# Kernel optimization log

Measured on AMD Instinct MI355X. Metric: run time of the kernel, lower is better.

## Reference

```python
import jax, jax.numpy as jnp
import numpy as np

B, S, M, E, H = 4, 2048, 1024, 8, 4096
CAP = 2 * (B * S) // E  # GShard top-2 capacity = 2*s/e = 2048


def setup_inputs() -> dict:
    key = jax.random.key(0)
    k = jax.random.split(key, 6)
    sc = 0.02
    return {
        "x": jax.random.normal(k[0], (B, S, M), jnp.float32),
        "wg": jax.random.normal(k[1], (M, E), jnp.float32) * sc,
        "w1": jax.random.normal(k[2], (E, M, H), jnp.float32) * sc,
        "b1": jnp.zeros((E, H), jnp.float32),
        "w2": jax.random.normal(k[3], (E, H, M), jnp.float32) * sc,
        "b2": jnp.zeros((E, M), jnp.float32),
    }


def top2gating(logits, capacity):
    # Faithful GShard/fairscale top2gating: logits [s, e]
    s, e = logits.shape
    gates = jax.nn.softmax(logits, axis=-1)
    idx1 = jnp.argmax(gates, axis=1)
    mask1 = jax.nn.one_hot(idx1, e, dtype=jnp.float32)
    logits2 = jnp.where(mask1 > 0, -jnp.inf, logits)
    idx2 = jnp.argmax(logits2, axis=1)
    mask2 = jax.nn.one_hot(idx2, e, dtype=jnp.float32)
    # positions within each expert's buffer
    loc1 = jnp.cumsum(mask1, axis=0) - 1.0
    loc2 = jnp.cumsum(mask2, axis=0) - 1.0 + jnp.sum(mask1, axis=0, keepdims=True)
    # load-balancing aux loss (computed before capacity drop, per fairscale)
    me = jnp.mean(gates, axis=0)
    ce = jnp.mean(mask1, axis=0)
    l_aux = jnp.mean(me * ce) * (e * e)
    # drop tokens over capacity
    mask1 = mask1 * (loc1 < capacity)
    mask2 = mask2 * (loc2 < capacity)
    loc1_s = jnp.sum(loc1 * mask1, axis=1).astype(jnp.int32)
    loc2_s = jnp.sum(loc2 * mask2, axis=1).astype(jnp.int32)
    gates1 = jnp.sum(gates * mask1, axis=1)
    gates2 = jnp.sum(gates * mask2, axis=1)
    denom = jnp.maximum(gates1 + gates2, 1e-9)
    gates1 = gates1 / denom
    gates2 = gates2 / denom
    # dense [s, e, c] combine weights (as in the original einsum formulation)
    oh1 = jax.nn.one_hot(loc1_s, capacity, dtype=jnp.float32)
    oh2 = jax.nn.one_hot(loc2_s, capacity, dtype=jnp.float32)
    combine = (gates1[:, None] * mask1)[:, :, None] * oh1[:, None, :] \
            + (gates2[:, None] * mask2)[:, :, None] * oh2[:, None, :]
    dispatch = combine > 0
    return l_aux, combine, dispatch


def reference(x, wg, w1, b1, w2, b2):
    d_model = x.shape[2]
    xf = x.reshape(-1, d_model)                      # [s, m]
    logits = xf @ wg                                 # [s, e]
    l_aux, combine, dispatch = top2gating(logits, CAP)
    # dispatch: dense one-hot scatter, as in torch.einsum('sec,sm->ecm')
    disp = jnp.einsum('sec,sm->ecm', dispatch.astype(xf.dtype), xf)
    # per-expert FFN (Linear -> ReLU -> Linear), vectorized over experts
    h = jax.nn.relu(jnp.einsum('ecm,emh->ech', disp, w1) + b1[:, None, :])
    eo = jnp.einsum('ech,ehm->ecm', h, w2) + b2[:, None, :]
    # combine: torch.einsum('sec,ecm->sm')
    out = jnp.einsum('sec,ecm->sm', combine, eo)
    return out.reshape(x.shape), l_aux
```

## Files before the change

kernel.cpp:

```cpp
#include <hip/hip_runtime.h>
#include <stdint.h>

typedef unsigned short u16;
typedef __attribute__((ext_vector_type(8))) short bf16x8;
typedef __attribute__((ext_vector_type(4))) float f32x4;

#define TOKENS 8192
#define DM 1024
#define NE 8
#define DH 4096
#define CAP 2048

__device__ __forceinline__ u16 f2bf(float f) {
  unsigned int u = __float_as_uint(f);
  u = u + 0x7FFFu + ((u >> 16) & 1u);
  return (u16)(u >> 16);
}

__device__ __forceinline__ void gll16(const void* g, void* l) {
  __builtin_amdgcn_global_load_lds(
      (const __attribute__((address_space(1))) unsigned int*)g,
      (__attribute__((address_space(3))) unsigned int*)l, 16, 0, 0);
}

__global__ __launch_bounds__(256) void gating_kernel(
    const float* __restrict__ x, const float* __restrict__ wg,
    int* __restrict__ idx1, int* __restrict__ idx2,
    float* __restrict__ g1r, float* __restrict__ g2r, float* __restrict__ me) {
  __shared__ float gsh[4][8];
  int lane = threadIdx.x & 63;
  int w = threadIdx.x >> 6;
  int t = blockIdx.x * 4 + w;
  const float* xr = x + (size_t)t * DM;
  double acc[8];
#pragma unroll
  for (int e = 0; e < 8; ++e) acc[e] = 0.0;
#pragma unroll
  for (int it = 0; it < 4; ++it) {
    float4 xv = ((const float4*)xr)[it * 64 + lane];
    int base = (it * 64 + lane) * 4;
    const float* wr = wg + (size_t)base * 8;
    float xs[4] = {xv.x, xv.y, xv.z, xv.w};
#pragma unroll
    for (int j = 0; j < 4; ++j)
#pragma unroll
      for (int e = 0; e < 8; ++e) acc[e] += (double)xs[j] * (double)wr[j * 8 + e];
  }
#pragma unroll
  for (int off = 32; off > 0; off >>= 1)
#pragma unroll
    for (int e = 0; e < 8; ++e) acc[e] += __shfl_down(acc[e], off);
  if (lane == 0) {
    float l[8];
#pragma unroll
    for (int e = 0; e < 8; ++e) l[e] = (float)acc[e];
    int i1 = 0;
    float v1 = l[0];
#pragma unroll
    for (int e = 1; e < 8; ++e)
      if (l[e] > v1) { v1 = l[e]; i1 = e; }
    int i2 = -1;
    float v2 = -3.4e38f;
#pragma unroll
    for (int e = 0; e < 8; ++e)
      if (e != i1 && l[e] > v2) { v2 = l[e]; i2 = e; }
    float s = 0.f;
    float p[8];
#pragma unroll
    for (int e = 0; e < 8; ++e) { p[e] = expf(l[e] - v1); s += p[e]; }
    float inv = 1.f / s;
    idx1[t] = i1;
    idx2[t] = i2;
    g1r[t] = inv;
    g2r[t] = expf(v2 - v1) * inv;
#pragma unroll
    for (int e = 0; e < 8; ++e) gsh[w][e] = p[e] * inv;
  }
  __syncthreads();
  if (threadIdx.x < 8) {
    int e = threadIdx.x;
    atomicAdd(&me[e], gsh[0][e] + gsh[1][e] + gsh[2][e] + gsh[3][e]);
  }
}

__global__ __launch_bounds__(1024) void scan_kernel(
    const int* __restrict__ idx1, const int* __restrict__ idx2,
    const float* __restrict__ g1r, const float* __restrict__ g2r,
    const float* __restrict__ me,
    int* __restrict__ slot1, int* __restrict__ slot2,
    float* __restrict__ g1n, float* __restrict__ g2n,
    int* __restrict__ slot2tok, float* __restrict__ laux) {
  __shared__ u16 c[16][1024];
  __shared__ u16 csum[16][32];
  __shared__ int tot[16];
  int tid = threadIdx.x;
  int i1[8], i2[8];
#pragma unroll
  for (int ctr = 0; ctr < 16; ++ctr) c[ctr][tid] = 0;
#pragma unroll
  for (int j = 0; j < 8; ++j) {
    int t = tid * 8 + j;
    i1[j] = idx1[t];
    i2[j] = idx2[t];
    c[i1[j]][tid]++;
    c[8 + i2[j]][tid]++;
  }
  __syncthreads();
  if (tid < 512) {
    int ctr = tid >> 5, ch = tid & 31;
    int s = 0;
#pragma unroll
    for (int i = 0; i < 32; ++i) s += c[ctr][ch * 32 + i];
    csum[ctr][ch] = (u16)s;
  }
  __syncthreads();
  if (tid < 16) {
    int run = 0;
#pragma unroll
    for (int ch = 0; ch < 32; ++ch) {
      int v = csum[tid][ch];
      csum[tid][ch] = (u16)run;
      run += v;
    }
    tot[tid] = run;
  }
  __syncthreads();
  if (tid < 512) {
    int ctr = tid >> 5, ch = tid & 31;
    int run = csum[ctr][ch];
#pragma unroll
    for (int i = 0; i < 32; ++i) {
      int v = c[ctr][ch * 32 + i];
      c[ctr][ch * 32 + i] = (u16)run;
      run += v;
    }
  }
  __syncthreads();
#pragma unroll
  for (int j = 0; j < 8; ++j) {
    int t = tid * 8 + j;
    int e1 = i1[j], e2 = i2[j];
    int L1 = c[e1][tid]++;
    int L2 = c[8 + e2][tid]++;
    L2 += tot[e2];
    bool kv1 = L1 < CAP, kv2 = L2 < CAP;
    float G1 = kv1 ? g1r[t] : 0.f;
    float G2 = kv2 ? g2r[t] : 0.f;
    float den = fmaxf(G1 + G2, 1e-9f);
    g1n[t] = G1 / den;
    g2n[t] = G2 / den;
    int s1 = kv1 ? (e1 * CAP + L1) : -1;
    int s2 = kv2 ? (e2 * CAP + L2) : -1;
    slot1[t] = s1;
    slot2[t] = s2;
    if (kv1) slot2tok[s1] = t;
    if (kv2) slot2tok[s2] = t;
  }
  if (tid == 0) {
    double a = 0.0;
    for (int e = 0; e < 8; ++e)
      a += ((double)me[e] / 8192.0) * ((double)tot[e] / 8192.0);
    laux[0] = (float)(a * 8.0);
  }
}

__global__ void transpose_kernel(const float* __restrict__ src, u16* __restrict__ dst,
                                 int R, int C) {
  __shared__ float tile[32][33];
  int tx = threadIdx.x, ty = threadIdx.y;
  int r0 = blockIdx.y * 32, c0 = blockIdx.x * 32;
  const float* s = src + (size_t)blockIdx.z * R * C;
  u16* d = dst + (size_t)blockIdx.z * R * C;
#pragma unroll
  for (int i = 0; i < 32; i += 8) tile[ty + i][tx] = s[(size_t)(r0 + ty + i) * C + c0 + tx];
  __syncthreads();
#pragma unroll
  for (int i = 0; i < 32; i += 8)
    d[(size_t)(c0 + ty + i) * R + r0 + tx] = f2bf(tile[tx][ty + i]);
}

__global__ void gather_kernel(const float* __restrict__ x, const int* __restrict__ slot2tok,
                              u16* __restrict__ xe) {
  int slot = blockIdx.y * CAP + blockIdx.x;
  int tok = slot2tok[slot];
  int tid = threadIdx.x;
  u16 o[8];
  if (tok >= 0) {
    const float4* xr = (const float4*)(x + (size_t)tok * DM);
    float4 a = xr[tid * 2], b = xr[tid * 2 + 1];
    o[0] = f2bf(a.x); o[1] = f2bf(a.y); o[2] = f2bf(a.z); o[3] = f2bf(a.w);
    o[4] = f2bf(b.x); o[5] = f2bf(b.y); o[6] = f2bf(b.z); o[7] = f2bf(b.w);
  } else {
#pragma unroll
    for (int j = 0; j < 8; ++j) o[j] = 0;
  }
  *(uint4*)(xe + (size_t)slot * DM + tid * 8) = *(const uint4*)o;
}

#define BAR()                              \
  {                                        \
    asm volatile("" ::: "memory");         \
    __builtin_amdgcn_s_barrier();          \
    asm volatile("" ::: "memory");         \
  }
#define VMCNT(n) asm volatile("s_waitcnt vmcnt(" #n ")" ::: "memory")

template <int RELU, int OUTBF16>
__global__ __launch_bounds__(512, 2) void gemm_kernel(
    const u16* __restrict__ A, const u16* __restrict__ Bt,
    const float* __restrict__ bias, void* __restrict__ Cv,
    int MO, int NO, int K) {
  __shared__ __align__(16) u16 As[2][256 * 64];
  __shared__ __align__(16) u16 Bs[2][256 * 64];
  const int tid = threadIdx.x;
  const int lane = tid & 63, wid = tid >> 6;
  const int wm = wid >> 2, wn = wid & 3;

  const int gx = gridDim.x, gy = gridDim.y;
  const int nwg = gx * gy * gridDim.z;
  const int L = (blockIdx.z * gy + blockIdx.y) * gx + blockIdx.x;
  const int cpx = nwg >> 3;
  const int Ls = (L & 7) * cpx + (L >> 3);
  const int bx = Ls % gx;
  const int tq = Ls / gx;
  const int by = tq % gy;
  const int eb = tq / gy;

  const size_t Ks2 = (size_t)K * 2;
  const char* Ag = (const char*)(A + (size_t)eb * MO * K + (size_t)by * 256 * K);
  const char* Bg = (const char*)(Bt + (size_t)eb * NO * K + (size_t)bx * 256 * K);
  const int rl = tid >> 3;
  const int sb = ((tid & 7) * 16) ^ ((rl & 7) << 4);
  Ag += (size_t)rl * Ks2 + sb;
  Bg += (size_t)rl * Ks2 + sb;
  char* AsB = ((char*)As) + tid * 16;
  char* BsB = ((char*)Bs) + tid * 16;
  const u16* AsE = &As[0][0];
  const u16* BsE = &Bs[0][0];
  const int fr = lane & 15, kg8 = (lane >> 4) * 8;
  const int swz = (fr & 7) << 3;

#define STAGE_A(BUF_, REG_, KT_) \
  gll16(Ag + (size_t)((REG_)*64) * Ks2 + (size_t)(KT_)*128, AsB + (BUF_)*32768 + (REG_)*8192)
#define STAGE_B(BUF_, REG_, KT_) \
  gll16(Bg + (size_t)((REG_)*64) * Ks2 + (size_t)(KT_)*128, BsB + (BUF_)*32768 + (REG_)*8192)
#define LDA(BUF_, M_, K_) \
  (*(const bf16x8*)&AsE[(BUF_)*16384 + (wm * 128 + (M_)*16 + fr) * 64 + (((K_)*32 + kg8) ^ swz)])
#define LDB(BUF_, N_, K_) \
  (*(const bf16x8*)&BsE[(BUF_)*16384 + (wn * 64 + (N_)*16 + fr) * 64 + (((K_)*32 + kg8) ^ swz)])
#define MFMA_Q(MB_, NB_)                                                            \
  _Pragma("unroll") for (int k = 0; k < 2; ++k)                                     \
  _Pragma("unroll") for (int m = 0; m < 4; ++m)                                     \
  _Pragma("unroll") for (int n = 0; n < 2; ++n)                                     \
      acc[(MB_) + m][(NB_) + n] = __builtin_amdgcn_mfma_f32_16x16x32_bf16(          \
          areg[m][k], breg[(NB_) + n][k], acc[(MB_) + m][(NB_) + n], 0, 0, 0)

  f32x4 acc[8][4];
#pragma unroll
  for (int i = 0; i < 8; ++i)
#pragma unroll
    for (int j = 0; j < 4; ++j) acc[i][j] = {0.f, 0.f, 0.f, 0.f};
  bf16x8 areg[4][2], breg[4][2];

  const int NT = K >> 6;

#define TILE_STEP(CUR_, NXT_, ST_)                                                  \
  {                                                                                 \
                          \
    STAGE_A(NXT_, 0, ST_); STAGE_A(NXT_, 1, ST_);                                   \
    STAGE_A(NXT_, 2, ST_); STAGE_A(NXT_, 3, ST_);                                   \
    STAGE_B(NXT_, 0, ST_); STAGE_B(NXT_, 1, ST_);                                   \
    STAGE_B(NXT_, 2, ST_); STAGE_B(NXT_, 3, ST_);                                   \
                                   \
    _Pragma("unroll") for (int m = 0; m < 4; ++m) {                                 \
      areg[m][0] = LDA(CUR_, m, 0); areg[m][1] = LDA(CUR_, m, 1);                   \
    }                                                                               \
    _Pragma("unroll") for (int n = 0; n < 4; ++n) {                                 \
      breg[n][0] = LDB(CUR_, n, 0); breg[n][1] = LDB(CUR_, n, 1);                   \
    }                                                                               \
    __builtin_amdgcn_s_setprio(1);                                                  \
    MFMA_Q(0, 0); MFMA_Q(0, 2);                                                     \
    __builtin_amdgcn_s_setprio(0);                                                  \
                          \
    _Pragma("unroll") for (int m = 0; m < 4; ++m) {                                 \
      areg[m][0] = LDA(CUR_, 4 + m, 0); areg[m][1] = LDA(CUR_, 4 + m, 1);           \
    }                                                                               \
    __builtin_amdgcn_s_setprio(1);                                                  \
    MFMA_Q(4, 0); MFMA_Q(4, 2);                                                     \
    __builtin_amdgcn_s_setprio(0);                                                  \
    VMCNT(0);           \
    BAR();              \
  }

  STAGE_A(0, 0, 0); STAGE_A(0, 1, 0); STAGE_A(0, 2, 0); STAGE_A(0, 3, 0);
  STAGE_B(0, 0, 0); STAGE_B(0, 1, 0); STAGE_B(0, 2, 0); STAGE_B(0, 3, 0);
  VMCNT(0);
  BAR();

  for (int t = 0; t < NT; t += 2) {
    const int s1 = (t + 1 < NT) ? t + 1 : NT - 1;
    const int s2 = (t + 2 < NT) ? t + 2 : NT - 1;
    TILE_STEP(0, 1, s1);
    TILE_STEP(1, 0, s2);
  }

  const int row0 = by * 256 + wm * 128 + (kg8 >> 3) * 4;
  const int col0 = bx * 256 + wn * 64 + fr;
  const float* be = bias + (size_t)eb * NO;
  size_t cbase = (size_t)eb * MO * NO;
#pragma unroll
  for (int m = 0; m < 8; ++m) {
#pragma unroll
    for (int n = 0; n < 4; ++n) {
      int col = col0 + n * 16;
      float bv = be[col];
#pragma unroll
      for (int r = 0; r < 4; ++r) {
        int row = row0 + m * 16 + r;
        float v = acc[m][n][r] + bv;
        if (RELU) v = fmaxf(v, 0.f);
        if (OUTBF16)
          ((u16*)Cv)[cbase + (size_t)row * NO + col] = f2bf(v);
        else
          ((float*)Cv)[cbase + (size_t)row * NO + col] = v;
      }
    }
  }
#undef TILE_STEP
#undef STAGE_A
#undef STAGE_B
#undef LDA
#undef LDB
#undef MFMA_Q
}

__global__ void combine_kernel(const float* __restrict__ eo,
                               const float* __restrict__ g1n, const float* __restrict__ g2n,
                               const int* __restrict__ slot1, const int* __restrict__ slot2,
                               float* __restrict__ out) {
  int t = blockIdx.x, tid = threadIdx.x;
  float g1 = g1n[t], g2 = g2n[t];
  int s1 = slot1[t], s2 = slot2[t];
  float4 o = make_float4(0.f, 0.f, 0.f, 0.f);
  if (s1 >= 0) {
    float4 a = ((const float4*)(eo + (size_t)s1 * DM))[tid];
    o.x = g1 * a.x; o.y = g1 * a.y; o.z = g1 * a.z; o.w = g1 * a.w;
  }
  if (s2 >= 0) {
    float4 b = ((const float4*)(eo + (size_t)s2 * DM))[tid];
    o.x += g2 * b.x; o.y += g2 * b.y; o.z += g2 * b.z; o.w += g2 * b.w;
  }
  ((float4*)(out + (size_t)t * DM))[tid] = o;
}

extern "C" void kernel_launch(void* const* d_in, const int* in_sizes, int n_in,
                              void* d_out, int out_size, void* d_ws, size_t ws_size,
                              hipStream_t stream) {
  const float* x = (const float*)d_in[0];
  const float* wg = (const float*)d_in[1];
  const float* w1 = (const float*)d_in[2];
  const float* b1 = (const float*)d_in[3];
  const float* w2 = (const float*)d_in[4];
  const float* b2 = (const float*)d_in[5];
  float* out = (float*)d_out;

  const size_t SZ_WT1 = (size_t)NE * DH * DM * 2;
  const size_t SZ_WT2 = (size_t)NE * DM * DH * 2;
  const size_t SZ_XE = (size_t)NE * CAP * DM * 2;
  const size_t SZ_H = (size_t)NE * CAP * DH * 2;
  const size_t SZ_TOK = (size_t)TOKENS * 4;

  char* p = (char*)d_ws;
  u16* wt1 = (u16*)p;
  float* eo = (float*)p;            p += SZ_WT1;
  u16* wt2 = (u16*)p;               p += SZ_WT2;
  u16* xe = (u16*)p;                p += SZ_XE;
  u16* h = (u16*)p;                 p += SZ_H;
  int* idx1 = (int*)p;              p += SZ_TOK;
  int* idx2 = (int*)p;              p += SZ_TOK;
  int* slot1 = (int*)p;             p += SZ_TOK;
  int* slot2 = (int*)p;             p += SZ_TOK;
  float* g1r = (float*)p;           p += SZ_TOK;
  float* g2r = (float*)p;           p += SZ_TOK;
  float* g1n = (float*)p;           p += SZ_TOK;
  float* g2n = (float*)p;           p += SZ_TOK;
  int* slot2tok = (int*)p;          p += (size_t)NE * CAP * 4;
  float* me = (float*)p;            p += 256;
  if ((size_t)(p - (char*)d_ws) > ws_size) return;

  hipMemsetAsync(me, 0, 32, stream);
  hipMemsetAsync(slot2tok, 0xFF, (size_t)NE * CAP * 4, stream);

  gating_kernel<<<TOKENS / 4, 256, 0, stream>>>(x, wg, idx1, idx2, g1r, g2r, me);
  scan_kernel<<<1, 1024, 0, stream>>>(idx1, idx2, g1r, g2r, me, slot1, slot2, g1n, g2n,
                                      slot2tok, out + (size_t)TOKENS * DM);
  transpose_kernel<<<dim3(DH / 32, DM / 32, NE), dim3(32, 8), 0, stream>>>(w1, wt1, DM, DH);
  transpose_kernel<<<dim3(DM / 32, DH / 32, NE), dim3(32, 8), 0, stream>>>(w2, wt2, DH, DM);
  gather_kernel<<<dim3(CAP, NE), 128, 0, stream>>>(x, slot2tok, xe);
  gemm_kernel<1, 1><<<dim3(DH / 256, CAP / 256, NE), 512, 0, stream>>>(xe, wt1, b1, (void*)h,
                                                                       CAP, DH, DM);
  gemm_kernel<0, 0><<<dim3(DM / 256, CAP / 256, NE), 512, 0, stream>>>(h, wt2, b2, (void*)eo,
                                                                       CAP, DM, DH);
  combine_kernel<<<TOKENS, 256, 0, stream>>>(eo, g1n, g2n, slot1, slot2, out);
}
```

Baseline: 461.6 us.

## Interleave global-to-LDS staging with MFMA quarters in a finer-grained ping-pong schedule

Replaces the per-tile stage-all-then-compute step with an 8-phase schedule. Each quarter of MFMA work is bracketed by barriers and lgkmcnt waits, and the next tile's A/B sub-blocks are issued piecewise between quarters. Part of the next buffer is prefetched up front, so global loads stay in flight across compute with partial vmcnt waits instead of a full drain each tile. This aims to hide load latency and smooth memory traffic, at the cost of many more barriers per tile and fragile hand-counted wait thresholds.

```diff
diff --git a/kernel.cpp b/kernel.cpp
--- a/kernel.cpp
+++ b/kernel.cpp
@@ -204,6 +204,7 @@
     asm volatile("" ::: "memory");         \
   }
 #define VMCNT(n) asm volatile("s_waitcnt vmcnt(" #n ")" ::: "memory")
+#define LGKM(n) asm volatile("s_waitcnt lgkmcnt(" #n ")" ::: "memory")
 
 template <int RELU, int OUTBF16>
 __global__ __launch_bounds__(512, 2) void gemm_kernel(
@@ -255,6 +256,31 @@
       acc[(MB_) + m][(NB_) + n] = __builtin_amdgcn_mfma_f32_16x16x32_bf16(          \
           areg[m][k], breg[(NB_) + n][k], acc[(MB_) + m][(NB_) + n], 0, 0, 0)
 
+#define RD_A03(C_)                                                \
+  _Pragma("unroll") for (int m = 0; m < 4; ++m) {                 \
+    areg[m][0] = LDA(C_, m, 0); areg[m][1] = LDA(C_, m, 1);       \
+  }
+#define RD_A47(C_)                                                \
+  _Pragma("unroll") for (int m = 0; m < 4; ++m) {                 \
+    areg[m][0] = LDA(C_, 4 + m, 0); areg[m][1] = LDA(C_, 4 + m, 1); \
+  }
+#define RD_B01(C_)                                                \
+  _Pragma("unroll") for (int n = 0; n < 2; ++n) {                 \
+    breg[n][0] = LDB(C_, n, 0); breg[n][1] = LDB(C_, n, 1);       \
+  }
+#define RD_B23(C_)                                                \
+  _Pragma("unroll") for (int n = 2; n < 4; ++n) {                 \
+    breg[n][0] = LDB(C_, n, 0); breg[n][1] = LDB(C_, n, 1);       \
+  }
+#define MM(MB_, NB_)                          \
+  BAR();                                      \
+  LGKM(0);                                    \
+  __builtin_amdgcn_sched_barrier(0);          \
+  __builtin_amdgcn_s_setprio(1);              \
+  MFMA_Q(MB_, NB_);                           \
+  __builtin_amdgcn_s_setprio(0);              \
+  BAR();
+
   f32x4 acc[8][4];
 #pragma unroll
   for (int i = 0; i < 8; ++i)
@@ -264,44 +290,43 @@
 
   const int NT = K >> 6;
 
-#define TILE_STEP(CUR_, NXT_, ST_)                                                  \
-  {                                                                                 \
-                          \
-    STAGE_A(NXT_, 0, ST_); STAGE_A(NXT_, 1, ST_);                                   \
-    STAGE_A(NXT_, 2, ST_); STAGE_A(NXT_, 3, ST_);                                   \
-    STAGE_B(NXT_, 0, ST_); STAGE_B(NXT_, 1, ST_);                                   \
-    STAGE_B(NXT_, 2, ST_); STAGE_B(NXT_, 3, ST_);                                   \
-                                   \
-    _Pragma("unroll") for (int m = 0; m < 4; ++m) {                                 \
-      areg[m][0] = LDA(CUR_, m, 0); areg[m][1] = LDA(CUR_, m, 1);                   \
-    }                                                                               \
-    _Pragma("unroll") for (int n = 0; n < 4; ++n) {                                 \
-      breg[n][0] = LDB(CUR_, n, 0); breg[n][1] = LDB(CUR_, n, 1);                   \
-    }                                                                               \
-    __builtin_amdgcn_s_setprio(1);                                                  \
-    MFMA_Q(0, 0); MFMA_Q(0, 2);                                                     \
-    __builtin_amdgcn_s_setprio(0);                                                  \
-                          \
-    _Pragma("unroll") for (int m = 0; m < 4; ++m) {                                 \
-      areg[m][0] = LDA(CUR_, 4 + m, 0); areg[m][1] = LDA(CUR_, 4 + m, 1);           \
-    }                                                                               \
-    __builtin_amdgcn_s_setprio(1);                                                  \
-    MFMA_Q(4, 0); MFMA_Q(4, 2);                                                     \
-    __builtin_amdgcn_s_setprio(0);                                                  \
-    VMCNT(0);           \
-    BAR();              \
-  }
-
   STAGE_A(0, 0, 0); STAGE_A(0, 1, 0); STAGE_A(0, 2, 0); STAGE_A(0, 3, 0);
   STAGE_B(0, 0, 0); STAGE_B(0, 1, 0); STAGE_B(0, 2, 0); STAGE_B(0, 3, 0);
-  VMCNT(0);
+  STAGE_A(1, 0, 1); STAGE_A(1, 2, 1);
+  STAGE_B(1, 0, 1); STAGE_B(1, 1, 1);
+  STAGE_B(1, 2, 1); STAGE_B(1, 3, 1);
+  VMCNT(6);
   BAR();
 
   for (int t = 0; t < NT; t += 2) {
-    const int s1 = (t + 1 < NT) ? t + 1 : NT - 1;
-    const int s2 = (t + 2 < NT) ? t + 2 : NT - 1;
-    TILE_STEP(0, 1, s1);
-    TILE_STEP(1, 0, s2);
+    const int t2 = (t + 2 < NT) ? t + 2 : NT - 2;
+    const int t3 = (t + 3 < NT) ? t + 3 : NT - 1;
+    RD_A03(0); RD_B01(0);
+    STAGE_A(1, 1, t + 1); STAGE_A(1, 3, t + 1);
+    LGKM(8);
+    MM(0, 0);
+    RD_B23(0);
+    STAGE_A(0, 0, t2); STAGE_A(0, 2, t2);
+    MM(0, 2);
+    RD_A47(0);
+    STAGE_B(0, 0, t2); STAGE_B(0, 1, t2);
+    MM(4, 0);
+    STAGE_B(0, 2, t2); STAGE_B(0, 3, t2);
+    VMCNT(6);
+    MM(4, 2);
+    RD_A03(1); RD_B01(1);
+    STAGE_A(0, 1, t2); STAGE_A(0, 3, t2);
+    LGKM(8);
+    MM(0, 0);
+    RD_B23(1);
+    STAGE_A(1, 0, t3); STAGE_A(1, 2, t3);
+    MM(0, 2);
+    RD_A47(1);
+    STAGE_B(1, 0, t3); STAGE_B(1, 1, t3);
+    MM(4, 0);
+    STAGE_B(1, 2, t3); STAGE_B(1, 3, t3);
+    VMCNT(6);
+    MM(4, 2);
   }
 
   const int row0 = by * 256 + wm * 128 + (kg8 >> 3) * 4;
@@ -326,7 +351,11 @@
       }
     }
   }
-#undef TILE_STEP
+#undef MM
+#undef RD_A03
+#undef RD_A47
+#undef RD_B01
+#undef RD_B23
 #undef STAGE_A
 #undef STAGE_B
 #undef LDA
```

New measurement: 471.6 us. 1.02x slower.
